# Kernel optimization log

Measured on AMD Instinct MI355X. Metric: run time of the kernel, lower is better.

Reference implementation:

```python
import jax, jax.numpy as jnp
import numpy as np

N = 50000        # nodes
E = 1600000      # edges (before self loops)
IN = 128         # in_channels
HID = 32         # hidden_channels
HEADS = 4
OUT = 16         # out_channels
B = 512          # graphs in batch
NEG_SLOPE = 0.2  # PyG GATConv default


def _uniform(key, shape, fan_in):
    s = 1.0 / np.sqrt(fan_in)
    return jax.random.uniform(key, shape, jnp.float32, -s, s)


def setup_inputs() -> dict:
    key = jax.random.key(0)
    ks = jax.random.split(key, 12)
    x = jax.random.normal(ks[0], (N, IN), jnp.float32)
    edge_index = jax.random.randint(ks[1], (2, E), 0, N, dtype=jnp.int64)
    batch = jnp.sort(jax.random.randint(ks[2], (N,), 0, B, dtype=jnp.int64))
    return {
        "x": x,
        "edge_index": edge_index,
        "batch": batch,
        "W1": _uniform(ks[3], (IN, HEADS * HID), IN),
        "att_src": _uniform(ks[4], (HEADS, HID), HID),
        "att_dst": _uniform(ks[5], (HEADS, HID), HID),
        "b1": jnp.zeros((HEADS * HID,), jnp.float32),
        "lin1_w": _uniform(ks[6], (HEADS * HID, HID), HEADS * HID),
        "lin1_b": _uniform(ks[7], (HID,), HEADS * HID),
        "lin2_w": _uniform(ks[8], (HID, OUT), HID),
        "lin2_b": _uniform(ks[9], (OUT,), HID),
    }


def _gat_conv(x, src, dst, W1, att_src, att_dst, b1):
    # h: [N, H, C]
    h = (x @ W1).reshape(N, HEADS, HID)
    a_s = (h * att_src).sum(-1)   # [N, H]
    a_d = (h * att_dst).sum(-1)   # [N, H]
    # per-edge attention logits [E', H]
    alpha = jax.nn.leaky_relu(a_s[src] + a_d[dst], negative_slope=NEG_SLOPE)
    # segment softmax over incoming edges of each destination node
    amax = jax.lax.stop_gradient(jax.ops.segment_max(alpha, dst, num_segments=N))
    ex = jnp.exp(alpha - amax[dst])
    den = jax.ops.segment_sum(ex, dst, num_segments=N)
    a = ex / (den[dst] + 1e-16)
    # weighted scatter-aggregate of source features: [N, H, C]
    out = jax.ops.segment_sum(h[src] * a[:, :, None], dst, num_segments=N)
    return out.reshape(N, HEADS * HID) + b1


def reference(x, edge_index, batch, W1, att_src, att_dst, b1, lin1_w, lin1_b, lin2_w, lin2_b):
    # add self loops (PyG GATConv default add_self_loops=True)
    loop = jnp.arange(N, dtype=edge_index.dtype)
    src = jnp.concatenate([edge_index[0], loop])
    dst = jnp.concatenate([edge_index[1], loop])
    # dropout layers are identity in eval mode
    xh = jax.nn.elu(_gat_conv(x, src, dst, W1, att_src, att_dst, b1))
    g = jax.ops.segment_sum(xh, batch, num_segments=B)  # global_add_pool -> [B, H*C]
    g = g @ lin1_w + lin1_b
    return g @ lin2_w + lin2_b
```

## Files before the change

kernel.cpp:

```cpp
#include <hip/hip_runtime.h>
#include <hip/hip_bf16.h>
#include <hip/hip_fp16.h>

#define N_NODES 50000
#define E_EDGES 1600000
#define IN_CH 128
#define HID 32
#define HEADS 4
#define HC (HEADS * HID)
#define OUT_CH 16
#define B_GRAPHS 512
#define NEG_SLOPE 0.2f
#define CAP 96
#define NB 512
#define BNODES 98
#define PCAP 3552
#define ACHUNK 4096
#define APART 391
#define ROWS_PB 64
#define GEMM_BLOCKS 782
#define TOT_BLOCKS 1173


typedef short bfrag __attribute__((ext_vector_type(8)));
typedef float facc  __attribute__((ext_vector_type(4)));

__device__ __forceinline__ unsigned short f2bf(float f) {
    unsigned int u = __float_as_uint(f);
    unsigned int r = (u + 0x7FFFu + ((u >> 16) & 1u)) >> 16;
    return (unsigned short)r;
}

__device__ __forceinline__ float lrelu_exp(float v) {
    v = v > 0.f ? v : NEG_SLOPE * v;
    return __expf(v);
}

__device__ __forceinline__ void split2(float a, float b,
                                       unsigned int& hi, unsigned int& lo) {
    unsigned int ua = __float_as_uint(a), ub = __float_as_uint(b);
    hi = (ua >> 16) | (ub & 0xFFFF0000u);
    float la = a - __uint_as_float(ua & 0xFFFF0000u);
    float lb = b - __uint_as_float(ub & 0xFFFF0000u);
    lo = (unsigned int)f2bf(la) | ((unsigned int)f2bf(lb) << 16);
}

__global__ __launch_bounds__(256) void k_prep(const float* __restrict__ W1,
                                              unsigned short* __restrict__ whiF,
                                              unsigned short* __restrict__ wloF,
                                              int* __restrict__ gcur) {
    int tid = blockIdx.x * 256 + threadIdx.x;
    if (tid < NB) gcur[tid] = 0;
    int e = tid & 7, l = (tid >> 3) & 63, q = tid >> 9;
    int nt = q >> 2, kc = q & 3;
    int n = nt * 16 + (l & 15);
    int k = kc * 32 + (l >> 4) * 8 + e;
    float v = W1[k * 128 + n];
    unsigned int u = __float_as_uint(v);
    float lo_f = v - __uint_as_float(u & 0xFFFF0000u);
    whiF[tid] = (unsigned short)(u >> 16);
    wloF[tid] = f2bf(lo_f);
}

__global__ __launch_bounds__(256) void k_fused(const float* __restrict__ x,
                                               const unsigned short* __restrict__ whiF,
                                               const unsigned short* __restrict__ wloF,
                                               const float* __restrict__ att_src,
                                               const float* __restrict__ att_dst,
                                               const int* __restrict__ ei,
                                               unsigned short* __restrict__ hb,
                                               float* __restrict__ a_s,
                                               float* __restrict__ a_d,
                                               int* __restrict__ gcur,
                                               unsigned int* __restrict__ ebuf,
                                               float* __restrict__ g) {
    __shared__ float smem[8256];
    const int t = threadIdx.x;
    const int bI = blockIdx.x;

    if (bI % 3 == 0) {
        const int ablk = bI / 3;
        int* scnt = (int*)smem;
        int* sbase = scnt + 4 * NB;
        const int wv = t >> 6;
        const int e0 = ablk * ACHUNK;
        int e1 = e0 + ACHUNK; if (e1 > E_EDGES) e1 = E_EDGES;
        for (int i = t; i < 4 * NB; i += 256) scnt[i] = 0;
        __syncthreads();
        const int* __restrict__ dstp = ei + E_EDGES;
        for (int e = e0 + t; e < e1; e += 256) {
            int d = dstp[e];
            atomicAdd(&scnt[wv * NB + d / BNODES], 1);
        }
        __syncthreads();
        for (int i = t; i < NB; i += 256) {
            int c0 = scnt[0 * NB + i], c1 = scnt[1 * NB + i];
            int c2 = scnt[2 * NB + i], c3 = scnt[3 * NB + i];
            int base = atomicAdd(&gcur[i], c0 + c1 + c2 + c3);
            sbase[0 * NB + i] = base;
            sbase[1 * NB + i] = base + c0;
            sbase[2 * NB + i] = base + c0 + c1;
            sbase[3 * NB + i] = base + c0 + c1 + c2;
            scnt[0 * NB + i] = 0; scnt[1 * NB + i] = 0;
            scnt[2 * NB + i] = 0; scnt[3 * NB + i] = 0;
        }
        __syncthreads();
        for (int e = e0 + t; e < e1; e += 256) {
            int d = dstp[e];
            int s = ei[e];
            int b = d / BNODES;
            int dl = d - b * BNODES;
            int pos = sbase[wv * NB + b] + atomicAdd(&scnt[wv * NB + b], 1);
            if (pos < PCAP)
                ebuf[(size_t)b * PCAP + pos] = ((unsigned int)dl << 16) | (unsigned int)s;
        }
        return;
    }

    const int bid = bI - bI / 3 - 1;
    const int n0 = bid * ROWS_PB;

    int gt = bid * 256 + t;
    if (gt < B_GRAPHS * HC) g[gt] = 0.f;

    unsigned short* swh = (unsigned short*)smem;
    {
        const uint4* wsrc = (const uint4*)whiF;
        uint4* wdst = (uint4*)swh;
#pragma unroll
        for (int it = 0; it < 8; it++)
            wdst[t + it * 256] = wsrc[t + it * 256];
    }

    const int wv = t >> 6, l = t & 63;
    const int lm = l & 15, lk = l >> 4;
    const int band = wv * 16;

    bfrag ahi[4], alo[4];
    {
        int row = n0 + band + lm;
        bool valid = row < N_NODES;
        const float* xr = x + (size_t)(valid ? row : 0) * IN_CH;
#pragma unroll
        for (int kc = 0; kc < 4; kc++) {
            float4 v0 = *(const float4*)(xr + kc * 32 + lk * 8);
            float4 v1 = *(const float4*)(xr + kc * 32 + lk * 8 + 4);
            if (!valid) { v0 = make_float4(0.f,0.f,0.f,0.f); v1 = v0; }
            union { bfrag f; unsigned int u[4]; } H, L;
            split2(v0.x, v0.y, H.u[0], L.u[0]);
            split2(v0.z, v0.w, H.u[1], L.u[1]);
            split2(v1.x, v1.y, H.u[2], L.u[2]);
            split2(v1.z, v1.w, H.u[3], L.u[3]);
            ahi[kc] = H.f; alo[kc] = L.f;
        }
    }

    facc acc[8];
#pragma unroll
    for (int nt = 0; nt < 8; nt++) acc[nt] = (facc){0.f, 0.f, 0.f, 0.f};

    __syncthreads();

    {
        const int lb = l * 8;
#pragma unroll
        for (int q = 0; q < 32; q++) {
            bfrag bhv = *(const bfrag*)(swh + q * 512 + lb);
            bfrag blv = *(const bfrag*)(wloF + q * 512 + lb);
            const int nt = q >> 2, kc = q & 3;
            acc[nt] = __builtin_amdgcn_mfma_f32_16x16x32_bf16(ahi[kc], bhv, acc[nt], 0, 0, 0);
            acc[nt] = __builtin_amdgcn_mfma_f32_16x16x32_bf16(alo[kc], bhv, acc[nt], 0, 0, 0);
            acc[nt] = __builtin_amdgcn_mfma_f32_16x16x32_bf16(ahi[kc], blv, acc[nt], 0, 0, 0);
        }
    }

    __syncthreads();
    float* sH = smem;
#pragma unroll
    for (int nt = 0; nt < 8; nt++) {
#pragma unroll
        for (int r = 0; r < 4; r++)
            sH[(band + lk * 4 + r) * 129 + nt * 16 + lm] = acc[nt][r];
    }
    __syncthreads();

    for (int i = t; i < 64 * 32; i += 256) {
        int row = i >> 5, c4 = i & 31;
        const float* p = &sH[row * 129 + c4 * 4];
        int n = n0 + row;
        if (n < N_NODES) {
            ushort4 o;
            o.x = f2bf(p[0]); o.y = f2bf(p[1]);
            o.z = f2bf(p[2]); o.w = f2bf(p[3]);
            *(ushort4*)&hb[(size_t)n * HC + c4 * 4] = o;
        }
    }

    if (t < 128) {
        int r = t & 63;
        int n = n0 + r;
        const float* __restrict__ av = (t < 64) ? att_src : att_dst;
        float s0 = 0.f, s1 = 0.f, s2 = 0.f, s3 = 0.f;
#pragma unroll 4
        for (int j = 0; j < 32; j++) {
            const float* row = &sH[r * 129 + j];
            s0 += row[0]  * av[j];
            s1 += row[32] * av[32 + j];
            s2 += row[64] * av[64 + j];
            s3 += row[96] * av[96 + j];
        }
        if (n < N_NODES) {
            float* dst = (t < 64) ? a_s : a_d;
            *(float4*)(dst + (size_t)n * 4) = make_float4(s0, s1, s2, s3);
        }
    }
}

#define NPW 7
__global__ __launch_bounds__(1024) void k_aggB(const unsigned int* __restrict__ ebuf,
                                               const int* __restrict__ gcur,
                                               const float* __restrict__ a_s,
                                               const float* __restrict__ a_d,
                                               const unsigned short* __restrict__ hb,
                                               const float* __restrict__ b1,
                                               const int* __restrict__ batch,
                                               float* __restrict__ g) {
    __shared__ unsigned short sbuf[BNODES * CAP];
    __shared__ int scnt[BNODES];
    __shared__ float sWt[16][4][97];
    const int t = threadIdx.x;
    const int b = blockIdx.x;
    const int dbase = b * BNODES;

    for (int i = t; i < BNODES; i += 1024) {
        int d = dbase + i;
        scnt[i] = (d < N_NODES) ? 1 : 0;
        sbuf[i * CAP] = (unsigned short)d;
    }
    __syncthreads();
    int m = gcur[b]; if (m > PCAP) m = PCAP;
    for (int i = t; i < m; i += 1024) {
        unsigned int p = ebuf[(size_t)b * PCAP + i];
        int dl = p >> 16;
        int s = p & 0xFFFFu;
        int c = atomicAdd(&scnt[dl], 1);
        if (c < CAP) sbuf[dl * CAP + c] = (unsigned short)s;
    }
    __syncthreads();

    const int wv = t >> 6;
    const int l = t & 63;
    const int head = l >> 4;
    const int c0 = 2 * l;
    int nl0 = wv * NPW;
    if (nl0 >= BNODES) return;
    int nl1 = nl0 + NPW; if (nl1 > BNODES) nl1 = BNODES;
    int gn0 = dbase + nl0;
    if (gn0 >= N_NODES) return;
    int gn1 = dbase + nl1; if (gn1 > N_NODES) gn1 = N_NODES;
    const float2 bias = *(const float2*)(b1 + c0);
    float pool0 = 0.f, pool1 = 0.f;
    int cur = batch[gn0];
    for (int n = gn0; n < gn1; n++) {
        int bb = batch[n];
        if (bb != cur) {
            atomicAdd(&g[(size_t)cur * HC + c0], pool0);
            atomicAdd(&g[(size_t)cur * HC + c0 + 1], pool1);
            pool0 = pool1 = 0.f;
            cur = bb;
        }
        int nl = n - dbase;
        int c = scnt[nl]; if (c > CAP) c = CAP;
        float4 ad = *(const float4*)(a_d + (size_t)n * 4);
        const unsigned short* __restrict__ srow = &sbuf[nl * CAP];
        for (int i = l; i < c; i += 64) {
            int s = srow[i];
            float4 as = *(const float4*)(a_s + (size_t)s * 4);
            sWt[wv][0][i] = lrelu_exp(as.x + ad.x);
            sWt[wv][1][i] = lrelu_exp(as.y + ad.y);
            sWt[wv][2][i] = lrelu_exp(as.z + ad.z);
            sWt[wv][3][i] = lrelu_exp(as.w + ad.w);
        }
        __asm__ volatile("" ::: "memory");
        const float* __restrict__ wrow = &sWt[wv][head][0];
        float acc0 = 0.f, acc1 = 0.f, dsum = 0.f;
        int i = 0;
        for (; i + 16 <= c; i += 16) {
            unsigned int u[16];
            float w[16];
#pragma unroll
            for (int q = 0; q < 16; q++) {
                int sq = srow[i + q];
                w[q] = wrow[i + q];
                u[q] = *(const unsigned int*)(hb + (size_t)sq * HC + c0);
            }
#pragma unroll
            for (int q = 0; q < 16; q++) {
                dsum += w[q];
                acc0 += w[q] * __uint_as_float(u[q] << 16);
                acc1 += w[q] * __uint_as_float(u[q] & 0xFFFF0000u);
            }
        }
        for (; i + 8 <= c; i += 8) {
            unsigned int u[8];
            float w[8];
#pragma unroll
            for (int q = 0; q < 8; q++) {
                int sq = srow[i + q];
                w[q] = wrow[i + q];
                u[q] = *(const unsigned int*)(hb + (size_t)sq * HC + c0);
            }
#pragma unroll
            for (int q = 0; q < 8; q++) {
                dsum += w[q];
                acc0 += w[q] * __uint_as_float(u[q] << 16);
                acc1 += w[q] * __uint_as_float(u[q] & 0xFFFF0000u);
            }
        }
        for (; i < c; i++) {
            int s0 = srow[i];
            float w0 = wrow[i];
            unsigned int u0 = *(const unsigned int*)(hb + (size_t)s0 * HC + c0);
            dsum += w0;
            acc0 += w0 * __uint_as_float(u0 << 16);
            acc1 += w0 * __uint_as_float(u0 & 0xFFFF0000u);
        }
        __asm__ volatile("" ::: "memory");
        float inv = 1.f / (dsum + 1e-16f);
        float v0 = acc0 * inv + bias.x; v0 = v0 > 0.f ? v0 : (__expf(v0) - 1.f);
        float v1 = acc1 * inv + bias.y; v1 = v1 > 0.f ? v1 : (__expf(v1) - 1.f);
        pool0 += v0;
        pool1 += v1;
    }
    atomicAdd(&g[(size_t)cur * HC + c0], pool0);
    atomicAdd(&g[(size_t)cur * HC + c0 + 1], pool1);
}

__global__ __launch_bounds__(64) void k_mlp(const float* __restrict__ g,
                                            const float* __restrict__ w1,
                                            const float* __restrict__ bb1,
                                            const float* __restrict__ w2,
                                            const float* __restrict__ bb2,
                                            float* __restrict__ out) {
    __shared__ float sg[HC];
    __shared__ float st[HID];
    int b = blockIdx.x;
    int t = threadIdx.x;
    sg[t]      = g[(size_t)b * HC + t];
    sg[t + 64] = g[(size_t)b * HC + 64 + t];
    __syncthreads();
    if (t < HID) {
        float acc = bb1[t];
#pragma unroll 8
        for (int k = 0; k < HC; k++) acc += sg[k] * w1[(size_t)k * HID + t];
        st[t] = acc;
    }
    __syncthreads();
    if (t < OUT_CH) {
        float acc = bb2[t];
#pragma unroll
        for (int k = 0; k < HID; k++) acc += st[k] * w2[(size_t)k * OUT_CH + t];
        out[(size_t)b * OUT_CH + t] = acc;
    }
}

extern "C" void kernel_launch(void* const* d_in, const int* in_sizes, int n_in,
                              void* d_out, int out_size, void* d_ws, size_t ws_size,
                              hipStream_t stream) {
    const float* x       = (const float*)d_in[0];
    const int*   ei      = (const int*)d_in[1];
    const int*   batch   = (const int*)d_in[2];
    const float* W1      = (const float*)d_in[3];
    const float* att_src = (const float*)d_in[4];
    const float* att_dst = (const float*)d_in[5];
    const float* b1      = (const float*)d_in[6];
    const float* lin1_w  = (const float*)d_in[7];
    const float* lin1_b  = (const float*)d_in[8];
    const float* lin2_w  = (const float*)d_in[9];
    const float* lin2_b  = (const float*)d_in[10];
    float* out = (float*)d_out;

    float* ws = (float*)d_ws;
    unsigned short* hb   = (unsigned short*)ws;
    float*  a_s      = ws + 3200000;
    float*  a_d      = ws + 3400000;
    unsigned int* ebuf = (unsigned int*)(ws + 3600000);
    unsigned short* whiF = (unsigned short*)(ws + 5418624);
    unsigned short* wloF = (unsigned short*)(ws + 5426816);
    int*    gcur     = (int*)(ws + 5435008);
    float*  g        = ws + 5436000;

    k_prep<<<64, 256, 0, stream>>>(W1, whiF, wloF, gcur);
    k_fused<<<TOT_BLOCKS, 256, 0, stream>>>(
        x, whiF, wloF, att_src, att_dst, ei, hb, a_s, a_d, gcur, ebuf, g);
    k_aggB<<<NB, 1024, 0, stream>>>(ebuf, gcur, a_s, a_d, hb, b1, batch, g);
    k_mlp<<<B_GRAPHS, 64, 0, stream>>>(g, lin1_w, lin1_b, lin2_w, lin2_b, out);
}
```

Measured before the change: 189.5 us.

## Compute attention dots in registers and stage bf16 tile in smaller shared memory

The GEMM blocks no longer copy the high-half weights into shared memory. They read them directly from global memory, which also drops one barrier. The per-node attention scores a_s and a_d are now computed from the MFMA accumulators with wavefront shuffle reductions, replacing the serial 128-thread loop over a shared-memory fp32 tile. The output tile is staged in shared memory as bf16, halving its footprint and the static shared allocation, which may raise occupancy; the cost is more global or L2 weight traffic per block and extra shuffle work.

```diff
diff --git a/kernel.cpp b/kernel.cpp
--- a/kernel.cpp
+++ b/kernel.cpp
@@ -74,7 +74,7 @@
                                                int* __restrict__ gcur,
                                                unsigned int* __restrict__ ebuf,
                                                float* __restrict__ g) {
-    __shared__ float smem[8256];
+    __shared__ float smem[4224];
     const int t = threadIdx.x;
     const int bI = blockIdx.x;
 
@@ -123,15 +123,6 @@
     int gt = bid * 256 + t;
     if (gt < B_GRAPHS * HC) g[gt] = 0.f;
 
-    unsigned short* swh = (unsigned short*)smem;
-    {
-        const uint4* wsrc = (const uint4*)whiF;
-        uint4* wdst = (uint4*)swh;
-#pragma unroll
-        for (int it = 0; it < 8; it++)
-            wdst[t + it * 256] = wsrc[t + it * 256];
-    }
-
     const int wv = t >> 6, l = t & 63;
     const int lm = l & 15, lk = l >> 4;
     const int band = wv * 16;
@@ -159,13 +150,11 @@
 #pragma unroll
     for (int nt = 0; nt < 8; nt++) acc[nt] = (facc){0.f, 0.f, 0.f, 0.f};
 
-    __syncthreads();
-
     {
         const int lb = l * 8;
 #pragma unroll
         for (int q = 0; q < 32; q++) {
-            bfrag bhv = *(const bfrag*)(swh + q * 512 + lb);
+            bfrag bhv = *(const bfrag*)(whiF + q * 512 + lb);
             bfrag blv = *(const bfrag*)(wloF + q * 512 + lb);
             const int nt = q >> 2, kc = q & 3;
             acc[nt] = __builtin_amdgcn_mfma_f32_16x16x32_bf16(ahi[kc], bhv, acc[nt], 0, 0, 0);
@@ -174,44 +163,51 @@
         }
     }
 
-    __syncthreads();
-    float* sH = smem;
+    {
+        float asv[8], adv[8];
+#pragma unroll
+        for (int nt = 0; nt < 8; nt++) {
+            asv[nt] = att_src[nt * 16 + lm];
+            adv[nt] = att_dst[nt * 16 + lm];
+        }
+#pragma unroll
+        for (int r = 0; r < 4; r++) {
+            float s[4], d4[4];
+#pragma unroll
+            for (int h = 0; h < 4; h++) {
+                s[h]  = acc[2*h][r] * asv[2*h] + acc[2*h+1][r] * asv[2*h+1];
+                d4[h] = acc[2*h][r] * adv[2*h] + acc[2*h+1][r] * adv[2*h+1];
+            }
+#pragma unroll
+            for (int m = 1; m < 16; m <<= 1) {
+#pragma unroll
+                for (int h = 0; h < 4; h++) {
+                    s[h]  += __shfl_xor(s[h], m);
+                    d4[h] += __shfl_xor(d4[h], m);
+                }
+            }
+            int n = n0 + band + lk * 4 + r;
+            if (lm == 0 && n < N_NODES) {
+                *(float4*)(a_s + (size_t)n * 4) = make_float4(s[0], s[1], s[2], s[3]);
+                *(float4*)(a_d + (size_t)n * 4) = make_float4(d4[0], d4[1], d4[2], d4[3]);
+            }
+        }
+    }
+
+    unsigned short* sHu = (unsigned short*)smem;
 #pragma unroll
     for (int nt = 0; nt < 8; nt++) {
 #pragma unroll
         for (int r = 0; r < 4; r++)
-            sH[(band + lk * 4 + r) * 129 + nt * 16 + lm] = acc[nt][r];
-    }
-    __syncthreads();
-
+            sHu[(band + lk * 4 + r) * 132 + nt * 16 + lm] = f2bf(acc[nt][r]);
+    }
+    __syncthreads();
     for (int i = t; i < 64 * 32; i += 256) {
         int row = i >> 5, c4 = i & 31;
-        const float* p = &sH[row * 129 + c4 * 4];
         int n = n0 + row;
         if (n < N_NODES) {
-            ushort4 o;
-            o.x = f2bf(p[0]); o.y = f2bf(p[1]);
-            o.z = f2bf(p[2]); o.w = f2bf(p[3]);
+            ushort4 o = *(const ushort4*)&sHu[row * 132 + c4 * 4];
             *(ushort4*)&hb[(size_t)n * HC + c4 * 4] = o;
-        }
-    }
-
-    if (t < 128) {
-        int r = t & 63;
-        int n = n0 + r;
-        const float* __restrict__ av = (t < 64) ? att_src : att_dst;
-        float s0 = 0.f, s1 = 0.f, s2 = 0.f, s3 = 0.f;
-#pragma unroll 4
-        for (int j = 0; j < 32; j++) {
-            const float* row = &sH[r * 129 + j];
-            s0 += row[0]  * av[j];
-            s1 += row[32] * av[32 + j];
-            s2 += row[64] * av[64 + j];
-            s3 += row[96] * av[96 + j];
-        }
-        if (n < N_NODES) {
-            float* dst = (t < 64) ? a_s : a_d;
-            *(float4*)(dst + (size_t)n * 4) = make_float4(s0, s1, s2, s3);
         }
     }
 }
```

After: 191.3 us. Within noise of the previous version (+1.0%).
